# Performance work log

Measured on AMD Instinct MI355X. Metric: run time of the kernel, lower is better.

## Reference

```python
import jax, jax.numpy as jnp
import numpy as np

N = 100000
E = 1_600_000
IN_DIM = 128
HIDDEN = 128


def spmm(row, col, vals, H):
    # y[r] = sum_{edges e with row[e]==r} vals[e] * H[col[e]]
    msgs = vals[:, None] * H[col]          # [E, hidden] gather + scale
    return jax.ops.segment_sum(msgs, row, num_segments=H.shape[0])


def setup_inputs() -> dict:
    key = jax.random.key(0)
    ks = jax.random.split(key, 10)
    X = jax.random.normal(ks[0], (N, IN_DIM), dtype=jnp.float32)
    row = jax.random.randint(ks[1], (E,), 0, N, dtype=jnp.int32)
    col = jax.random.randint(ks[2], (E,), 0, N, dtype=jnp.int32)
    vals = jax.random.uniform(ks[3], (E,), dtype=jnp.float32)
    s_in = 1.0 / np.sqrt(IN_DIM)
    s_h = 1.0 / np.sqrt(HIDDEN)
    W_in = jax.random.normal(ks[4], (IN_DIM, HIDDEN), dtype=jnp.float32) * s_in
    b_in = jax.random.normal(ks[5], (HIDDEN,), dtype=jnp.float32) * s_in
    W_mp1 = jax.random.normal(ks[6], (HIDDEN, HIDDEN), dtype=jnp.float32) * s_h
    W_mp2 = jax.random.normal(ks[7], (HIDDEN, HIDDEN), dtype=jnp.float32) * s_h
    W_out = jax.random.normal(ks[8], (HIDDEN, 1), dtype=jnp.float32) * s_h
    b_out = jax.random.normal(ks[9], (1,), dtype=jnp.float32) * s_h
    return {"X": X, "row": row, "col": col, "vals": vals,
            "W_in": W_in, "b_in": b_in, "W_mp1": W_mp1, "W_mp2": W_mp2,
            "W_out": W_out, "b_out": b_out}


def reference(X, row, col, vals, W_in, b_in, W_mp1, W_mp2, W_out, b_out):
    H = jax.nn.relu(X @ W_in + b_in)          # [N, hidden]
    AH = spmm(row, col, vals, H)              # 1-hop propagation
    A2H = spmm(row, col, vals, AH)            # 2-hop propagation
    H2 = jax.nn.relu(AH @ W_mp1 + A2H @ W_mp2)
    return H2 @ W_out + b_out                 # [N, 1]
```

## Files before the change

### kernel.cpp

```cpp
#include <hip/hip_runtime.h>

#define N_NODES 100000
#define N_EDGES 1600000
#define NBUCK 391
#define NCHUNK 256
#define CHUNK 6250
#define LROW 136
#define DCAP 5120

typedef float f32x4 __attribute__((ext_vector_type(4)));
typedef _Float16 f16x8 __attribute__((ext_vector_type(8)));
typedef _Float16 h16x2 __attribute__((ext_vector_type(2)));

__device__ __forceinline__ unsigned f2h_bits(float f) {
    union { _Float16 h; unsigned short s; } c;
    c.h = (_Float16)f;
    return c.s;
}
__device__ __forceinline__ h16x2 u2h(unsigned u) {
    union { unsigned u; h16x2 h; } c;
    c.u = u;
    return c.h;
}
__device__ __forceinline__ unsigned pk16lo(unsigned hi, unsigned lo) {
    return __builtin_amdgcn_perm(hi, lo, 0x05040100u);
}
__device__ __forceinline__ unsigned pk16hi(unsigned hi, unsigned lo) {
    return __builtin_amdgcn_perm(hi, lo, 0x07060302u);
}
__device__ __forceinline__ float fdot2(h16x2 a, h16x2 b, float c) {
#if __has_builtin(__builtin_amdgcn_fdot2)
    return __builtin_amdgcn_fdot2(a, b, c, false);
#else
    return c + (float)a[0] * (float)b[0] + (float)a[1] * (float)b[1];
#endif
}

__device__ __forceinline__ f16x8 pack_h8(float4 a, float4 b) {
    f16x8 r;
    r[0] = (_Float16)a.x; r[1] = (_Float16)a.y;
    r[2] = (_Float16)a.z; r[3] = (_Float16)a.w;
    r[4] = (_Float16)b.x; r[5] = (_Float16)b.y;
    r[6] = (_Float16)b.z; r[7] = (_Float16)b.w;
    return r;
}


__global__ __launch_bounds__(256) void k_prep(const int* __restrict__ row,
                                              int* __restrict__ hmat,
                                              const float* __restrict__ Wa,
                                              const float* __restrict__ Wb,
                                              const float* __restrict__ Wc,
                                              unsigned short* __restrict__ Wta,
                                              unsigned short* __restrict__ Wtb,
                                              unsigned short* __restrict__ Wtc) {
    if (blockIdx.x < NCHUNK) {
        __shared__ int h[NBUCK];
        for (int i = threadIdx.x; i < NBUCK; i += 256) h[i] = 0;
        __syncthreads();
        int s = blockIdx.x * CHUNK, e = s + CHUNK;
        for (int i = s + threadIdx.x; i < e; i += 256)
            atomicAdd(&h[row[i] >> 8], 1);
        __syncthreads();
        for (int b = threadIdx.x; b < NBUCK; b += 256)
            hmat[blockIdx.x * NBUCK + b] = h[b];
    } else {
        int t = (blockIdx.x - NCHUNK) * 256 + threadIdx.x;
        int which = t >> 14;
        int i = t & 16383;
        int n = i & 127, k = i >> 7;
        const float* W = which == 0 ? Wa : which == 1 ? Wb : Wc;
        unsigned short* Wt = which == 0 ? Wta : which == 1 ? Wtb : Wtc;
        Wt[n * 128 + k] = (unsigned short)f2h_bits(W[k * 128 + n]);
    }
}

__global__ __launch_bounds__(512) void k_colscanB(const int* __restrict__ hmat,
                                                  int* __restrict__ bases,
                                                  int* __restrict__ bstart) {
    __shared__ int s[512];
    int b = blockIdx.x, t = threadIdx.x;
    if (b < NBUCK) {
        int v = (t < NCHUNK) ? hmat[t * NBUCK + b] : 0;
        s[t] = v;
        __syncthreads();
        for (int off = 1; off < 512; off <<= 1) {
            int x = (t >= off) ? s[t - off] : 0;
            __syncthreads();
            s[t] += x;
            __syncthreads();
        }
        if (t < NCHUNK) bases[t * NBUCK + b] = s[t] - v;
    } else {
        int v = 0;
        if (t < NBUCK) {
            for (int blk = 0; blk < NCHUNK; blk++) v += hmat[blk * NBUCK + t];
        }
        s[t] = v;
        __syncthreads();
        for (int off = 1; off < 512; off <<= 1) {
            int x = (t >= off) ? s[t - off] : 0;
            __syncthreads();
            s[t] += x;
            __syncthreads();
        }
        if (t < NBUCK) bstart[t] = s[t] - v;
        if (t == NBUCK) bstart[NBUCK] = N_EDGES;
    }
}

__global__ __launch_bounds__(256) void k_binC_gemm(const int* __restrict__ row,
                                                   const int* __restrict__ col,
                                                   const float* __restrict__ vals,
                                                   const int* __restrict__ bstart,
                                                   const int* __restrict__ bases,
                                                   int2* __restrict__ grouped,
                                                   const float* __restrict__ X,
                                                   const unsigned short* __restrict__ Wt,
                                                   const float* __restrict__ bvec,
                                                   unsigned short* __restrict__ H) {
    __shared__ __align__(16) char smraw[64 * LROW * 2];
    if (blockIdx.x < NCHUNK) {
        int* cnt = (int*)smraw;
        int* basl = (int*)(smraw + 1600);
        for (int i = threadIdx.x; i < NBUCK; i += 256) {
            cnt[i] = 0;
            basl[i] = bstart[i] + bases[blockIdx.x * NBUCK + i];
        }
        __syncthreads();
        int s = blockIdx.x * CHUNK, e = s + CHUNK;
        for (int i = s + threadIdx.x; i < e; i += 256) {
            int r = row[i];
            int b = r >> 8;
            int rank = atomicAdd(&cnt[b], 1);
            int pos = basl[b] + rank;
            unsigned hv = f2h_bits(vals[i]);
            grouped[pos] = make_int2(col[i], ((r & 255) << 14) | hv);
        }
    } else {
        unsigned short* lds = (unsigned short*)smraw;
        int tid = threadIdx.x;
        int lane = tid & 63, wv = tid >> 6;
        int quad = lane >> 4, c16 = lane & 15;

        f16x8 wf[2][4];
        float bb[2];
#pragma unroll
        for (int nt = 0; nt < 2; nt++) {
            int ng = wv * 2 + nt;
            bb[nt] = bvec[ng * 16 + c16];
#pragma unroll
            for (int kc = 0; kc < 4; kc++)
                wf[nt][kc] = *(const f16x8*)&Wt[(ng * 16 + c16) * 128 + kc * 32 + quad * 8];
        }

        int tilebase = (blockIdx.x - NCHUNK) * 64;
        const float4* Xg = (const float4*)X;
#pragma unroll
        for (int i = 0; i < 4; i++) {
            int c = tid + i * 256;
            int r = c >> 4, o = c & 15;
            int grow = tilebase + r;
            float4 f0 = make_float4(0.f, 0.f, 0.f, 0.f), f1 = f0;
            if (grow < N_NODES) {
                f0 = Xg[(size_t)grow * 32 + o * 2];
                f1 = Xg[(size_t)grow * 32 + o * 2 + 1];
            }
            *(f16x8*)&lds[r * LROW + o * 8] = pack_h8(f0, f1);
        }
        __syncthreads();

        f32x4 acc[4][2] = {};
#pragma unroll
        for (int t4 = 0; t4 < 4; t4++) {
#pragma unroll
            for (int kc = 0; kc < 4; kc++) {
                f16x8 af = *(const f16x8*)&lds[(t4 * 16 + c16) * LROW + kc * 32 + quad * 8];
#pragma unroll
                for (int nt = 0; nt < 2; nt++)
                    acc[t4][nt] = __builtin_amdgcn_mfma_f32_16x16x32_f16(af, wf[nt][kc],
                                                                        acc[t4][nt], 0, 0, 0);
            }
        }
        __syncthreads();

#pragma unroll
        for (int t4 = 0; t4 < 4; t4++)
#pragma unroll
            for (int nt = 0; nt < 2; nt++) {
                int ncol = (wv * 2 + nt) * 16 + c16;
#pragma unroll
                for (int r = 0; r < 4; r++) {
                    float v = fmaxf(acc[t4][nt][r] + bb[nt], 0.f);
                    lds[(t4 * 16 + quad * 4 + r) * LROW + ncol] = (unsigned short)f2h_bits(v);
                }
            }
        __syncthreads();
#pragma unroll
        for (int i = 0; i < 4; i++) {
            int c = tid + i * 256;
            int r = c >> 4, o = c & 15;
            int grow = tilebase + r;
            if (grow < N_NODES)
                *(uint4*)&H[(size_t)grow * 128 + o * 8] = *(const uint4*)&lds[r * LROW + o * 8];
        }
    }
}

__global__ __launch_bounds__(512) void k_binD(const int2* __restrict__ grouped,
                                              const int* __restrict__ bstart,
                                              unsigned* __restrict__ evf,
                                              int* __restrict__ row_ptr) {
    __shared__ int h[256], sc[256], cur[256];
    __shared__ int2 ebuf[DCAP];
    int b = blockIdx.x, t = threadIdx.x;
    int s0 = bstart[b], e0 = bstart[b + 1];
    int n = e0 - s0;
    bool inlds = (n <= DCAP);
    if (t < 256) h[t] = 0;
    __syncthreads();
    if (inlds) {
        for (int i = t; i < n; i += 512) ebuf[i] = grouped[s0 + i];
        __syncthreads();
        for (int i = t; i < n; i += 512)
            atomicAdd(&h[(ebuf[i].y >> 14) & 255], 1);
    } else {
        for (int i = s0 + t; i < e0; i += 512)
            atomicAdd(&h[(grouped[i].y >> 14) & 255], 1);
    }
    __syncthreads();
    int v = 0;
    if (t < 256) {
        v = h[t];
        sc[t] = v;
    }
    __syncthreads();
    for (int off = 1; off < 256; off <<= 1) {
        int x = (t >= off && t < 256) ? sc[t - off] : 0;
        __syncthreads();
        if (t < 256) sc[t] += x;
        __syncthreads();
    }
    if (t < 256) {
        int excl = sc[t] - v;
        cur[t] = excl;
        int grow = b * 256 + t;
        if (grow <= N_NODES) row_ptr[grow] = s0 + excl;
    }
    __syncthreads();
    if (inlds) {
        for (int i = t; i < n; i += 512) {
            int2 g = ebuf[i];
            int rl = (g.y >> 14) & 255;
            int p = atomicAdd(&cur[rl], 1);
            evf[s0 + p] = ((unsigned)g.x << 14) | (unsigned)(g.y & 0x3fff);
        }
    } else {
        for (int i = s0 + t; i < e0; i += 512) {
            int2 g = grouped[i];
            int rl = (g.y >> 14) & 255;
            int p = atomicAdd(&cur[rl], 1);
            evf[s0 + p] = ((unsigned)g.x << 14) | (unsigned)(g.y & 0x3fff);
        }
    }
}

#define STEP16(EV, R, A0, A1, A2, A3, A4, A5, A6, A7)                          \
    do {                                                                       \
        unsigned u0 = __shfl(EV, (R) + q, 64);                                 \
        unsigned u1 = __shfl(EV, (R) + 4 + q, 64);                             \
        unsigned u2 = __shfl(EV, (R) + 8 + q, 64);                             \
        unsigned u3 = __shfl(EV, (R) + 12 + q, 64);                            \
        const uint4 h0 = *(const uint4*)&Hin[(size_t)(u0 >> 14) * 64 + l16 * 4]; \
        const uint4 h1 = *(const uint4*)&Hin[(size_t)(u1 >> 14) * 64 + l16 * 4]; \
        const uint4 h2 = *(const uint4*)&Hin[(size_t)(u2 >> 14) * 64 + l16 * 4]; \
        const uint4 h3 = *(const uint4*)&Hin[(size_t)(u3 >> 14) * 64 + l16 * 4]; \
        h16x2 v01 = u2h(pk16lo(u1 & 0x3fffu, u0 & 0x3fffu));                   \
        h16x2 v23 = u2h(pk16lo(u3 & 0x3fffu, u2 & 0x3fffu));                   \
        A0 = fdot2(v01, u2h(pk16lo(h1.x, h0.x)), A0);                          \
        A0 = fdot2(v23, u2h(pk16lo(h3.x, h2.x)), A0);                          \
        A1 = fdot2(v01, u2h(pk16hi(h1.x, h0.x)), A1);                          \
        A1 = fdot2(v23, u2h(pk16hi(h3.x, h2.x)), A1);                          \
        A2 = fdot2(v01, u2h(pk16lo(h1.y, h0.y)), A2);                          \
        A2 = fdot2(v23, u2h(pk16lo(h3.y, h2.y)), A2);                          \
        A3 = fdot2(v01, u2h(pk16hi(h1.y, h0.y)), A3);                          \
        A3 = fdot2(v23, u2h(pk16hi(h3.y, h2.y)), A3);                          \
        A4 = fdot2(v01, u2h(pk16lo(h1.z, h0.z)), A4);                          \
        A4 = fdot2(v23, u2h(pk16lo(h3.z, h2.z)), A4);                          \
        A5 = fdot2(v01, u2h(pk16hi(h1.z, h0.z)), A5);                          \
        A5 = fdot2(v23, u2h(pk16hi(h3.z, h2.z)), A5);                          \
        A6 = fdot2(v01, u2h(pk16lo(h1.w, h0.w)), A6);                          \
        A6 = fdot2(v23, u2h(pk16lo(h3.w, h2.w)), A6);                          \
        A7 = fdot2(v01, u2h(pk16hi(h1.w, h0.w)), A7);                          \
        A7 = fdot2(v23, u2h(pk16hi(h3.w, h2.w)), A7);                          \
    } while (0)

__global__ __launch_bounds__(256) void k_spmm(const int* __restrict__ rp,
                                              const unsigned* __restrict__ evf,
                                              const unsigned* __restrict__ Hin,
                                              unsigned* __restrict__ Ho) {
    int tid = threadIdx.x;
    int lane = tid & 63;
    int q = lane >> 4, l16 = lane & 15;
    int wid = (blockIdx.x * 256 + tid) >> 6;
    int rA = wid * 2;
    int sA = __builtin_amdgcn_readfirstlane(rp[rA]);
    int eA = __builtin_amdgcn_readfirstlane(rp[rA + 1]);
    int eB = __builtin_amdgcn_readfirstlane(rp[rA + 2]);
    int sB = eA;
    float aA0 = 0.f, aA1 = 0.f, aA2 = 0.f, aA3 = 0.f;
    float aA4 = 0.f, aA5 = 0.f, aA6 = 0.f, aA7 = 0.f;
    float aB0 = 0.f, aB1 = 0.f, aB2 = 0.f, aB3 = 0.f;
    float aB4 = 0.f, aB5 = 0.f, aB6 = 0.f, aB7 = 0.f;
    int baseA = sA, baseB = sB;
    while (baseA < eA || baseB < eB) {
        int cntA = eA - baseA;
        if (cntA > 64) cntA = 64;
        if (cntA < 0) cntA = 0;
        int cntB = eB - baseB;
        if (cntB > 64) cntB = 64;
        if (cntB < 0) cntB = 0;
        unsigned evA = 0u, evB = 0u;
        if (cntA) {
            evA = evf[baseA + (lane < cntA ? lane : cntA - 1)];
            if (lane >= cntA) evA &= ~0x3fffu;
        }
        if (cntB) {
            evB = evf[baseB + (lane < cntB ? lane : cntB - 1)];
            if (lane >= cntB) evB &= ~0x3fffu;
        }
        int cm = cntA > cntB ? cntA : cntB;
        for (int r = 0; r < cm; r += 16) {
            if (r < cntA) STEP16(evA, r, aA0, aA1, aA2, aA3, aA4, aA5, aA6, aA7);
            if (r < cntB) STEP16(evB, r, aB0, aB1, aB2, aB3, aB4, aB5, aB6, aB7);
        }
        baseA += cntA;
        baseB += cntB;
    }
    aA0 += __shfl_xor(aA0, 16, 64); aA0 += __shfl_xor(aA0, 32, 64);
    aA1 += __shfl_xor(aA1, 16, 64); aA1 += __shfl_xor(aA1, 32, 64);
    aA2 += __shfl_xor(aA2, 16, 64); aA2 += __shfl_xor(aA2, 32, 64);
    aA3 += __shfl_xor(aA3, 16, 64); aA3 += __shfl_xor(aA3, 32, 64);
    aA4 += __shfl_xor(aA4, 16, 64); aA4 += __shfl_xor(aA4, 32, 64);
    aA5 += __shfl_xor(aA5, 16, 64); aA5 += __shfl_xor(aA5, 32, 64);
    aA6 += __shfl_xor(aA6, 16, 64); aA6 += __shfl_xor(aA6, 32, 64);
    aA7 += __shfl_xor(aA7, 16, 64); aA7 += __shfl_xor(aA7, 32, 64);
    aB0 += __shfl_xor(aB0, 16, 64); aB0 += __shfl_xor(aB0, 32, 64);
    aB1 += __shfl_xor(aB1, 16, 64); aB1 += __shfl_xor(aB1, 32, 64);
    aB2 += __shfl_xor(aB2, 16, 64); aB2 += __shfl_xor(aB2, 32, 64);
    aB3 += __shfl_xor(aB3, 16, 64); aB3 += __shfl_xor(aB3, 32, 64);
    aB4 += __shfl_xor(aB4, 16, 64); aB4 += __shfl_xor(aB4, 32, 64);
    aB5 += __shfl_xor(aB5, 16, 64); aB5 += __shfl_xor(aB5, 32, 64);
    aB6 += __shfl_xor(aB6, 16, 64); aB6 += __shfl_xor(aB6, 32, 64);
    aB7 += __shfl_xor(aB7, 16, 64); aB7 += __shfl_xor(aB7, 32, 64);
    if (q < 2) {
        float r0 = q ? aB0 : aA0, r1 = q ? aB1 : aA1;
        float r2 = q ? aB2 : aA2, r3 = q ? aB3 : aA3;
        float r4 = q ? aB4 : aA4, r5 = q ? aB5 : aA5;
        float r6 = q ? aB6 : aA6, r7 = q ? aB7 : aA7;
        uint4 p;
        p.x = (f2h_bits(r1) << 16) | f2h_bits(r0);
        p.y = (f2h_bits(r3) << 16) | f2h_bits(r2);
        p.z = (f2h_bits(r5) << 16) | f2h_bits(r4);
        p.w = (f2h_bits(r7) << 16) | f2h_bits(r6);
        *(uint4*)&Ho[(size_t)(rA + q) * 64 + l16 * 4] = p;
    }
}

__global__ __launch_bounds__(256) void k_gemm_out(const unsigned short* __restrict__ AH,
                                                  const unsigned short* __restrict__ A2H,
                                                  const unsigned short* __restrict__ Wt1,
                                                  const unsigned short* __restrict__ Wt2,
                                                  const float* __restrict__ Wout,
                                                  const float* __restrict__ bout,
                                                  float* __restrict__ out) {
    __shared__ unsigned short lds[2][64 * LROW];
    __shared__ float part[4][64];
    int tid = threadIdx.x;
    int lane = tid & 63, wv = tid >> 6;
    int quad = lane >> 4, c16 = lane & 15;

    f16x8 w1f[2][4], w2f[2][4];
    float wo[2];
#pragma unroll
    for (int nt = 0; nt < 2; nt++) {
        int ng = wv * 2 + nt;
        wo[nt] = Wout[ng * 16 + c16];
#pragma unroll
        for (int kc = 0; kc < 4; kc++) {
            w1f[nt][kc] = *(const f16x8*)&Wt1[(ng * 16 + c16) * 128 + kc * 32 + quad * 8];
            w2f[nt][kc] = *(const f16x8*)&Wt2[(ng * 16 + c16) * 128 + kc * 32 + quad * 8];
        }
    }
    float bo = bout[0];

    int tilebase = blockIdx.x * 64;
    const uint4* Ag = (const uint4*)(AH + (size_t)tilebase * 128);
    const uint4* Bg = (const uint4*)(A2H + (size_t)tilebase * 128);
#pragma unroll
    for (int i = 0; i < 4; i++) {
        int c = tid + i * 256;
        int r = c >> 4, o = c & 15;
        *(uint4*)&lds[0][r * LROW + o * 8] = Ag[c];
        *(uint4*)&lds[1][r * LROW + o * 8] = Bg[c];
    }
    __syncthreads();

    f32x4 acc[4][2] = {};
#pragma unroll
    for (int t4 = 0; t4 < 4; t4++) {
#pragma unroll
        for (int kc = 0; kc < 4; kc++) {
            f16x8 afA = *(const f16x8*)&lds[0][(t4 * 16 + c16) * LROW + kc * 32 + quad * 8];
            f16x8 afB = *(const f16x8*)&lds[1][(t4 * 16 + c16) * LROW + kc * 32 + quad * 8];
#pragma unroll
            for (int nt = 0; nt < 2; nt++) {
                acc[t4][nt] = __builtin_amdgcn_mfma_f32_16x16x32_f16(afA, w1f[nt][kc],
                                                                    acc[t4][nt], 0, 0, 0);
                acc[t4][nt] = __builtin_amdgcn_mfma_f32_16x16x32_f16(afB, w2f[nt][kc],
                                                                    acc[t4][nt], 0, 0, 0);
            }
        }
    }

#pragma unroll
    for (int t4 = 0; t4 < 4; t4++) {
        float p[4];
#pragma unroll
        for (int r = 0; r < 4; r++)
            p[r] = fmaxf(acc[t4][0][r], 0.f) * wo[0] + fmaxf(acc[t4][1][r], 0.f) * wo[1];
#pragma unroll
        for (int m = 1; m < 16; m <<= 1)
#pragma unroll
            for (int r = 0; r < 4; r++) p[r] += __shfl_xor(p[r], m, 64);
        if (c16 == 0)
#pragma unroll
            for (int r = 0; r < 4; r++) part[wv][t4 * 16 + quad * 4 + r] = p[r];
    }
    __syncthreads();
    if (tid < 64) {
        int orow = tilebase + tid;
        if (orow < N_NODES)
            out[orow] = part[0][tid] + part[1][tid] + part[2][tid] + part[3][tid] + bo;
    }
}


extern "C" void kernel_launch(void* const* d_in, const int* in_sizes, int n_in,
                              void* d_out, int out_size, void* d_ws, size_t ws_size,
                              hipStream_t stream) {
    const float* X    = (const float*)d_in[0];
    const int*   row  = (const int*)d_in[1];
    const int*   col  = (const int*)d_in[2];
    const float* vals = (const float*)d_in[3];
    const float* W_in = (const float*)d_in[4];
    const float* b_in = (const float*)d_in[5];
    const float* W1   = (const float*)d_in[6];
    const float* W2   = (const float*)d_in[7];
    const float* Wout = (const float*)d_in[8];
    const float* bout = (const float*)d_in[9];
    float* out = (float*)d_out;

    char* ws = (char*)d_ws;
    size_t off = 0;
    auto alloc = [&](size_t bytes) -> void* {
        void* p = ws + off;
        off += (bytes + 511) & ~(size_t)511;
        return p;
    };
    unsigned short* Hb  = (unsigned short*)alloc((size_t)N_NODES * 128 * 2);
    unsigned short* AHb = (unsigned short*)alloc((size_t)N_NODES * 128 * 2);
    unsigned short* A2b = (unsigned short*)alloc((size_t)N_NODES * 128 * 2);
    unsigned* evf  = (unsigned*)alloc((size_t)N_EDGES * 4);
    int2* grouped  = (int2*)alloc((size_t)N_EDGES * 8);
    unsigned short* Wtin = (unsigned short*)alloc(128 * 128 * 2);
    unsigned short* Wt1  = (unsigned short*)alloc(128 * 128 * 2);
    unsigned short* Wt2  = (unsigned short*)alloc(128 * 128 * 2);
    int*   hmat    = (int*)alloc((size_t)NCHUNK * NBUCK * 4);
    int*   bases   = (int*)alloc((size_t)NCHUNK * NBUCK * 4);
    int*   bstart  = (int*)alloc(512 * 4);
    int*   row_ptr = (int*)alloc((size_t)(N_NODES + 256) * 4);

    int gblk = (N_NODES + 63) / 64;

    k_prep<<<NCHUNK + 192, 256, 0, stream>>>(row, hmat, W_in, W1, W2, Wtin, Wt1, Wt2);
    k_colscanB<<<NBUCK + 1, 512, 0, stream>>>(hmat, bases, bstart);
    k_binC_gemm<<<NCHUNK + gblk, 256, 0, stream>>>(row, col, vals, bstart, bases,
                                                   grouped, X, Wtin, b_in, Hb);
    k_binD<<<NBUCK, 512, 0, stream>>>(grouped, bstart, evf, row_ptr);

    int sblk = N_NODES / 8;
    k_spmm<<<sblk, 256, 0, stream>>>(row_ptr, evf, (const unsigned*)Hb, (unsigned*)AHb);
    k_spmm<<<sblk, 256, 0, stream>>>(row_ptr, evf, (const unsigned*)AHb, (unsigned*)A2b);

    k_gemm_out<<<gblk, 256, 0, stream>>>(AHb, A2b, Wt1, Wt2, Wout, bout, out);
}
```

Measured before the change: 307.0 us.

## Process four rows per wavefront in SpMM with batched gathers before dots

The SpMM kernel now assigns four destination rows to each wavefront instead of two, and issues all sixteen gathers for the four rows before doing any dot products. This exposes more memory-level parallelism per wave to hide gather latency, and lets all four quarter-wave groups store output. It adds register pressure (32 accumulators plus 16 uint4 loads) under a 4-waves-per-SIMD launch bound. Padded lanes now load zero edge words, which point at node 0 with zero weight, so those lanes gather that row and add nothing.

```diff
diff --git a/kernel.cpp b/kernel.cpp
--- a/kernel.cpp
+++ b/kernel.cpp
@@ -265,77 +265,94 @@
     }
 }
 
-#define STEP16(EV, R, A0, A1, A2, A3, A4, A5, A6, A7)                          \
-    do {                                                                       \
-        unsigned u0 = __shfl(EV, (R) + q, 64);                                 \
-        unsigned u1 = __shfl(EV, (R) + 4 + q, 64);                             \
-        unsigned u2 = __shfl(EV, (R) + 8 + q, 64);                             \
-        unsigned u3 = __shfl(EV, (R) + 12 + q, 64);                            \
-        const uint4 h0 = *(const uint4*)&Hin[(size_t)(u0 >> 14) * 64 + l16 * 4]; \
-        const uint4 h1 = *(const uint4*)&Hin[(size_t)(u1 >> 14) * 64 + l16 * 4]; \
-        const uint4 h2 = *(const uint4*)&Hin[(size_t)(u2 >> 14) * 64 + l16 * 4]; \
-        const uint4 h3 = *(const uint4*)&Hin[(size_t)(u3 >> 14) * 64 + l16 * 4]; \
-        h16x2 v01 = u2h(pk16lo(u1 & 0x3fffu, u0 & 0x3fffu));                   \
-        h16x2 v23 = u2h(pk16lo(u3 & 0x3fffu, u2 & 0x3fffu));                   \
-        A0 = fdot2(v01, u2h(pk16lo(h1.x, h0.x)), A0);                          \
-        A0 = fdot2(v23, u2h(pk16lo(h3.x, h2.x)), A0);                          \
-        A1 = fdot2(v01, u2h(pk16hi(h1.x, h0.x)), A1);                          \
-        A1 = fdot2(v23, u2h(pk16hi(h3.x, h2.x)), A1);                          \
-        A2 = fdot2(v01, u2h(pk16lo(h1.y, h0.y)), A2);                          \
-        A2 = fdot2(v23, u2h(pk16lo(h3.y, h2.y)), A2);                          \
-        A3 = fdot2(v01, u2h(pk16hi(h1.y, h0.y)), A3);                          \
-        A3 = fdot2(v23, u2h(pk16hi(h3.y, h2.y)), A3);                          \
-        A4 = fdot2(v01, u2h(pk16lo(h1.z, h0.z)), A4);                          \
-        A4 = fdot2(v23, u2h(pk16lo(h3.z, h2.z)), A4);                          \
-        A5 = fdot2(v01, u2h(pk16hi(h1.z, h0.z)), A5);                          \
-        A5 = fdot2(v23, u2h(pk16hi(h3.z, h2.z)), A5);                          \
-        A6 = fdot2(v01, u2h(pk16lo(h1.w, h0.w)), A6);                          \
-        A6 = fdot2(v23, u2h(pk16lo(h3.w, h2.w)), A6);                          \
-        A7 = fdot2(v01, u2h(pk16hi(h1.w, h0.w)), A7);                          \
-        A7 = fdot2(v23, u2h(pk16hi(h3.w, h2.w)), A7);                          \
-    } while (0)
-
-__global__ __launch_bounds__(256) void k_spmm(const int* __restrict__ rp,
-                                              const unsigned* __restrict__ evf,
-                                              const unsigned* __restrict__ Hin,
-                                              unsigned* __restrict__ Ho) {
+#define GATH(EV, H0, H1, H2, H3, V01, V23)                                     \
+    {                                                                          \
+        unsigned u0 = __shfl(EV, r + q, 64);                                   \
+        unsigned u1 = __shfl(EV, r + 4 + q, 64);                               \
+        unsigned u2 = __shfl(EV, r + 8 + q, 64);                               \
+        unsigned u3 = __shfl(EV, r + 12 + q, 64);                              \
+        H0 = *(const uint4*)&Hin[(size_t)(u0 >> 14) * 64 + l16 * 4];           \
+        H1 = *(const uint4*)&Hin[(size_t)(u1 >> 14) * 64 + l16 * 4];           \
+        H2 = *(const uint4*)&Hin[(size_t)(u2 >> 14) * 64 + l16 * 4];           \
+        H3 = *(const uint4*)&Hin[(size_t)(u3 >> 14) * 64 + l16 * 4];           \
+        V01 = u2h(pk16lo(u1 & 0x3fffu, u0 & 0x3fffu));                         \
+        V23 = u2h(pk16lo(u3 & 0x3fffu, u2 & 0x3fffu));                         \
+    }
+
+#define DOT16(H0, H1, H2, H3, V01, V23, A0, A1, A2, A3, A4, A5, A6, A7)        \
+    {                                                                          \
+        A0 = fdot2(V01, u2h(pk16lo(H1.x, H0.x)), A0);                          \
+        A0 = fdot2(V23, u2h(pk16lo(H3.x, H2.x)), A0);                          \
+        A1 = fdot2(V01, u2h(pk16hi(H1.x, H0.x)), A1);                          \
+        A1 = fdot2(V23, u2h(pk16hi(H3.x, H2.x)), A1);                          \
+        A2 = fdot2(V01, u2h(pk16lo(H1.y, H0.y)), A2);                          \
+        A2 = fdot2(V23, u2h(pk16lo(H3.y, H2.y)), A2);                          \
+        A3 = fdot2(V01, u2h(pk16hi(H1.y, H0.y)), A3);                          \
+        A3 = fdot2(V23, u2h(pk16hi(H3.y, H2.y)), A3);                          \
+        A4 = fdot2(V01, u2h(pk16lo(H1.z, H0.z)), A4);                          \
+        A4 = fdot2(V23, u2h(pk16lo(H3.z, H2.z)), A4);                          \
+        A5 = fdot2(V01, u2h(pk16hi(H1.z, H0.z)), A5);                          \
+        A5 = fdot2(V23, u2h(pk16hi(H3.z, H2.z)), A5);                          \
+        A6 = fdot2(V01, u2h(pk16lo(H1.w, H0.w)), A6);                          \
+        A6 = fdot2(V23, u2h(pk16lo(H3.w, H2.w)), A6);                          \
+        A7 = fdot2(V01, u2h(pk16hi(H1.w, H0.w)), A7);                          \
+        A7 = fdot2(V23, u2h(pk16hi(H3.w, H2.w)), A7);                          \
+    }
+
+__global__ __launch_bounds__(256, 4) void k_spmm(const int* __restrict__ rp,
+                                                 const unsigned* __restrict__ evf,
+                                                 const unsigned* __restrict__ Hin,
+                                                 unsigned* __restrict__ Ho) {
     int tid = threadIdx.x;
     int lane = tid & 63;
     int q = lane >> 4, l16 = lane & 15;
     int wid = (blockIdx.x * 256 + tid) >> 6;
-    int rA = wid * 2;
-    int sA = __builtin_amdgcn_readfirstlane(rp[rA]);
-    int eA = __builtin_amdgcn_readfirstlane(rp[rA + 1]);
-    int eB = __builtin_amdgcn_readfirstlane(rp[rA + 2]);
-    int sB = eA;
+    int r0 = wid * 4;
+    int b0 = __builtin_amdgcn_readfirstlane(rp[r0]);
+    int b1 = __builtin_amdgcn_readfirstlane(rp[r0 + 1]);
+    int b2 = __builtin_amdgcn_readfirstlane(rp[r0 + 2]);
+    int b3 = __builtin_amdgcn_readfirstlane(rp[r0 + 3]);
+    int b4 = __builtin_amdgcn_readfirstlane(rp[r0 + 4]);
+    int baseA = b0, endA = b1;
+    int baseB = b1, endB = b2;
+    int baseC = b2, endC = b3;
+    int baseD = b3, endD = b4;
     float aA0 = 0.f, aA1 = 0.f, aA2 = 0.f, aA3 = 0.f;
     float aA4 = 0.f, aA5 = 0.f, aA6 = 0.f, aA7 = 0.f;
     float aB0 = 0.f, aB1 = 0.f, aB2 = 0.f, aB3 = 0.f;
     float aB4 = 0.f, aB5 = 0.f, aB6 = 0.f, aB7 = 0.f;
-    int baseA = sA, baseB = sB;
-    while (baseA < eA || baseB < eB) {
-        int cntA = eA - baseA;
-        if (cntA > 64) cntA = 64;
-        if (cntA < 0) cntA = 0;
-        int cntB = eB - baseB;
-        if (cntB > 64) cntB = 64;
-        if (cntB < 0) cntB = 0;
-        unsigned evA = 0u, evB = 0u;
-        if (cntA) {
-            evA = evf[baseA + (lane < cntA ? lane : cntA - 1)];
-            if (lane >= cntA) evA &= ~0x3fffu;
-        }
-        if (cntB) {
-            evB = evf[baseB + (lane < cntB ? lane : cntB - 1)];
-            if (lane >= cntB) evB &= ~0x3fffu;
-        }
-        int cm = cntA > cntB ? cntA : cntB;
+    float aC0 = 0.f, aC1 = 0.f, aC2 = 0.f, aC3 = 0.f;
+    float aC4 = 0.f, aC5 = 0.f, aC6 = 0.f, aC7 = 0.f;
+    float aD0 = 0.f, aD1 = 0.f, aD2 = 0.f, aD3 = 0.f;
+    float aD4 = 0.f, aD5 = 0.f, aD6 = 0.f, aD7 = 0.f;
+    for (;;) {
+        int cA = endA - baseA; cA = cA < 0 ? 0 : (cA > 64 ? 64 : cA);
+        int cB = endB - baseB; cB = cB < 0 ? 0 : (cB > 64 ? 64 : cB);
+        int cC = endC - baseC; cC = cC < 0 ? 0 : (cC > 64 ? 64 : cC);
+        int cD = endD - baseD; cD = cD < 0 ? 0 : (cD > 64 ? 64 : cD);
+        int cm = cA > cB ? cA : cB;
+        if (cC > cm) cm = cC;
+        if (cD > cm) cm = cD;
+        if (cm == 0) break;
+        unsigned evA = 0u, evB = 0u, evC = 0u, evD = 0u;
+        if (lane < cA) evA = evf[baseA + lane];
+        if (lane < cB) evB = evf[baseB + lane];
+        if (lane < cC) evC = evf[baseC + lane];
+        if (lane < cD) evD = evf[baseD + lane];
         for (int r = 0; r < cm; r += 16) {
-            if (r < cntA) STEP16(evA, r, aA0, aA1, aA2, aA3, aA4, aA5, aA6, aA7);
-            if (r < cntB) STEP16(evB, r, aB0, aB1, aB2, aB3, aB4, aB5, aB6, aB7);
-        }
-        baseA += cntA;
-        baseB += cntB;
+            uint4 hA0, hA1, hA2, hA3, hB0, hB1, hB2, hB3;
+            uint4 hC0, hC1, hC2, hC3, hD0, hD1, hD2, hD3;
+            h16x2 vA01, vA23, vB01, vB23, vC01, vC23, vD01, vD23;
+            GATH(evA, hA0, hA1, hA2, hA3, vA01, vA23);
+            GATH(evB, hB0, hB1, hB2, hB3, vB01, vB23);
+            GATH(evC, hC0, hC1, hC2, hC3, vC01, vC23);
+            GATH(evD, hD0, hD1, hD2, hD3, vD01, vD23);
+            DOT16(hA0, hA1, hA2, hA3, vA01, vA23, aA0, aA1, aA2, aA3, aA4, aA5, aA6, aA7);
+            DOT16(hB0, hB1, hB2, hB3, vB01, vB23, aB0, aB1, aB2, aB3, aB4, aB5, aB6, aB7);
+            DOT16(hC0, hC1, hC2, hC3, vC01, vC23, aC0, aC1, aC2, aC3, aC4, aC5, aC6, aC7);
+            DOT16(hD0, hD1, hD2, hD3, vD01, vD23, aD0, aD1, aD2, aD3, aD4, aD5, aD6, aD7);
+        }
+        baseA += cA; baseB += cB; baseC += cC; baseD += cD;
     }
     aA0 += __shfl_xor(aA0, 16, 64); aA0 += __shfl_xor(aA0, 32, 64);
     aA1 += __shfl_xor(aA1, 16, 64); aA1 += __shfl_xor(aA1, 32, 64);
@@ -353,18 +370,36 @@
     aB5 += __shfl_xor(aB5, 16, 64); aB5 += __shfl_xor(aB5, 32, 64);
     aB6 += __shfl_xor(aB6, 16, 64); aB6 += __shfl_xor(aB6, 32, 64);
     aB7 += __shfl_xor(aB7, 16, 64); aB7 += __shfl_xor(aB7, 32, 64);
-    if (q < 2) {
-        float r0 = q ? aB0 : aA0, r1 = q ? aB1 : aA1;
-        float r2 = q ? aB2 : aA2, r3 = q ? aB3 : aA3;
-        float r4 = q ? aB4 : aA4, r5 = q ? aB5 : aA5;
-        float r6 = q ? aB6 : aA6, r7 = q ? aB7 : aA7;
-        uint4 p;
-        p.x = (f2h_bits(r1) << 16) | f2h_bits(r0);
-        p.y = (f2h_bits(r3) << 16) | f2h_bits(r2);
-        p.z = (f2h_bits(r5) << 16) | f2h_bits(r4);
-        p.w = (f2h_bits(r7) << 16) | f2h_bits(r6);
-        *(uint4*)&Ho[(size_t)(rA + q) * 64 + l16 * 4] = p;
-    }
+    aC0 += __shfl_xor(aC0, 16, 64); aC0 += __shfl_xor(aC0, 32, 64);
+    aC1 += __shfl_xor(aC1, 16, 64); aC1 += __shfl_xor(aC1, 32, 64);
+    aC2 += __shfl_xor(aC2, 16, 64); aC2 += __shfl_xor(aC2, 32, 64);
+    aC3 += __shfl_xor(aC3, 16, 64); aC3 += __shfl_xor(aC3, 32, 64);
+    aC4 += __shfl_xor(aC4, 16, 64); aC4 += __shfl_xor(aC4, 32, 64);
+    aC5 += __shfl_xor(aC5, 16, 64); aC5 += __shfl_xor(aC5, 32, 64);
+    aC6 += __shfl_xor(aC6, 16, 64); aC6 += __shfl_xor(aC6, 32, 64);
+    aC7 += __shfl_xor(aC7, 16, 64); aC7 += __shfl_xor(aC7, 32, 64);
+    aD0 += __shfl_xor(aD0, 16, 64); aD0 += __shfl_xor(aD0, 32, 64);
+    aD1 += __shfl_xor(aD1, 16, 64); aD1 += __shfl_xor(aD1, 32, 64);
+    aD2 += __shfl_xor(aD2, 16, 64); aD2 += __shfl_xor(aD2, 32, 64);
+    aD3 += __shfl_xor(aD3, 16, 64); aD3 += __shfl_xor(aD3, 32, 64);
+    aD4 += __shfl_xor(aD4, 16, 64); aD4 += __shfl_xor(aD4, 32, 64);
+    aD5 += __shfl_xor(aD5, 16, 64); aD5 += __shfl_xor(aD5, 32, 64);
+    aD6 += __shfl_xor(aD6, 16, 64); aD6 += __shfl_xor(aD6, 32, 64);
+    aD7 += __shfl_xor(aD7, 16, 64); aD7 += __shfl_xor(aD7, 32, 64);
+    float s0 = q == 0 ? aA0 : q == 1 ? aB0 : q == 2 ? aC0 : aD0;
+    float s1 = q == 0 ? aA1 : q == 1 ? aB1 : q == 2 ? aC1 : aD1;
+    float s2 = q == 0 ? aA2 : q == 1 ? aB2 : q == 2 ? aC2 : aD2;
+    float s3 = q == 0 ? aA3 : q == 1 ? aB3 : q == 2 ? aC3 : aD3;
+    float s4 = q == 0 ? aA4 : q == 1 ? aB4 : q == 2 ? aC4 : aD4;
+    float s5 = q == 0 ? aA5 : q == 1 ? aB5 : q == 2 ? aC5 : aD5;
+    float s6 = q == 0 ? aA6 : q == 1 ? aB6 : q == 2 ? aC6 : aD6;
+    float s7 = q == 0 ? aA7 : q == 1 ? aB7 : q == 2 ? aC7 : aD7;
+    uint4 p;
+    p.x = (f2h_bits(s1) << 16) | f2h_bits(s0);
+    p.y = (f2h_bits(s3) << 16) | f2h_bits(s2);
+    p.z = (f2h_bits(s5) << 16) | f2h_bits(s4);
+    p.w = (f2h_bits(s7) << 16) | f2h_bits(s6);
+    *(uint4*)&Ho[(size_t)(r0 + q) * 64 + l16 * 4] = p;
 }
 
 __global__ __launch_bounds__(256) void k_gemm_out(const unsigned short* __restrict__ AH,
@@ -489,7 +524,7 @@
                                                    grouped, X, Wtin, b_in, Hb);
     k_binD<<<NBUCK, 512, 0, stream>>>(grouped, bstart, evf, row_ptr);
 
-    int sblk = N_NODES / 8;
+    int sblk = N_NODES / 16;
     k_spmm<<<sblk, 256, 0, stream>>>(row_ptr, evf, (const unsigned*)Hb, (unsigned*)AHb);
     k_spmm<<<sblk, 256, 0, stream>>>(row_ptr, evf, (const unsigned*)AHb, (unsigned*)A2b);
 
```

Result: no change. 308.2 us (+0.4%).
